# Kernel optimization log

Measured on AMD Instinct MI355X. Metric: run time of the kernel, lower is better.

Reference implementation:

```python
import jax, jax.numpy as jnp
import numpy as np

N = 100000      # n_nodes
D = 64          # in_features == out_features (elementwise W mul requires equality)
DEG = 16        # avg degree for random edges
H = 2           # n_head
ALPHA = 0.2     # LeakyReLU negative slope


def setup_inputs() -> dict:
    key = jax.random.key(0)
    k1, k2, k3 = jax.random.split(key, 3)
    inputs = jax.random.normal(k1, (N, D), dtype=jnp.float32)
    # random edges + self-loops so every row has at least one edge (nonzero rowsum)
    rnd = jax.random.randint(k2, (2, N * DEG), 0, N)
    self_loops = jnp.tile(jnp.arange(N)[None, :], (2, 1))
    edge_index = jnp.concatenate([self_loops, rnd], axis=1)  # [2, 1.7M]
    # per-head params, matching torch init: W = ones, a ~ U(-stdv, stdv)
    W = jnp.ones((H, D), dtype=jnp.float32)
    stdv = 1.0 / np.sqrt(D * 2)
    a = jax.random.uniform(k3, (H, 2 * D), dtype=jnp.float32, minval=-stdv, maxval=stdv)
    return {"inputs": inputs, "edge_index": edge_index, "W": W, "a": a}


def reference(inputs, edge_index, W, a):
    n = inputs.shape[0]
    row, col = edge_index[0], edge_index[1]

    def head(Wh, ah):
        h = inputs * Wh  # [N, D]
        # a @ [h_src; h_dst] decomposes into per-node dots, then scalar edge gather
        score = (h @ ah[:D])[row] + (h @ ah[D:])[col]          # [E]
        e = jnp.exp(jnp.where(score > 0, score, ALPHA * score))  # exp(leaky_relu)
        rowsum = jax.ops.segment_sum(e, row, num_segments=n)     # [N]
        # sparse.mm(coo(edge, e), inputs): h_prime[i] = sum_j e_ij * inputs[j]
        h_prime = jax.ops.segment_sum(e[:, None] * inputs[col], row, num_segments=n)
        return h_prime / rowsum[:, None]

    outs = jax.vmap(head)(W, a)  # [H, N, D]
    return outs.mean(axis=0)
```

## Files before the change

kernel.cpp:

```cpp
#include <hip/hip_runtime.h>


#define D 64
#define ALPHA 0.2f
#define CAP 96
#define BSHIFT 9
#define BROWS 512
#define MAXBUK 256
#define TILE 2048
#define PACKSHIFT 23
#define COLMASK ((1u << PACKSHIFT) - 1u)

__device__ __forceinline__ unsigned bf16rne(float f) {
    unsigned u = __float_as_uint(f);
    u += 0x7fffu + ((u >> 16) & 1u);
    return u >> 16;
}

__global__ __launch_bounds__(256) void k_scores_cast(
    const float* __restrict__ x, const float* __restrict__ W,
    const float* __restrict__ a, float4* __restrict__ s,
    unsigned short* __restrict__ xh, int N)
{
    int wid  = (blockIdx.x * blockDim.x + threadIdx.x) >> 6;
    int lane = threadIdx.x & 63;
    if (wid >= N) return;
    float v = x[(size_t)wid * D + lane];
    xh[(size_t)wid * D + lane] = (unsigned short)bf16rne(v);
    float h0 = v * W[lane];
    float h1 = v * W[D + lane];
    float t0 = h0 * a[lane];
    float t1 = h0 * a[D + lane];
    float t2 = h1 * a[2 * D + lane];
    float t3 = h1 * a[3 * D + lane];
#pragma unroll
    for (int off = 32; off; off >>= 1) {
        t0 += __shfl_xor(t0, off);
        t1 += __shfl_xor(t1, off);
        t2 += __shfl_xor(t2, off);
        t3 += __shfl_xor(t3, off);
    }
    if (lane == 0) s[wid] = make_float4(t0, t1, t2, t3);
}

__global__ __launch_bounds__(256) void k_tile_hist(
    const int* __restrict__ row, unsigned short* __restrict__ tcnt, int E, int nbuk)
{
    __shared__ int h[MAXBUK];
    int t = threadIdx.x, base = blockIdx.x * TILE;
    int cnt = E - base; if (cnt > TILE) cnt = TILE;
    for (int i = t; i < nbuk; i += 256) h[i] = 0;
    __syncthreads();
    for (int i = t; i < cnt; i += 256) atomicAdd(&h[row[base + i] >> BSHIFT], 1);
    __syncthreads();
    for (int i = t; i < nbuk; i += 256)
        tcnt[(size_t)blockIdx.x * MAXBUK + i] = (unsigned short)h[i];
}

__global__ __launch_bounds__(256) void k_col_scan(
    const unsigned short* __restrict__ tcnt, int* __restrict__ tbase,
    int* __restrict__ bcnt, int NT, int nbuk)
{
    __shared__ int wsum[256];
    int b = blockIdx.x, t = threadIdx.x;
    int t4 = t * 4;
    int v0 = (t4     < NT) ? tcnt[(size_t)(t4    ) * MAXBUK + b] : 0;
    int v1 = (t4 + 1 < NT) ? tcnt[(size_t)(t4 + 1) * MAXBUK + b] : 0;
    int v2 = (t4 + 2 < NT) ? tcnt[(size_t)(t4 + 2) * MAXBUK + b] : 0;
    int v3 = (t4 + 3 < NT) ? tcnt[(size_t)(t4 + 3) * MAXBUK + b] : 0;
    int sv = v0 + v1 + v2 + v3;
    wsum[t] = sv;
    __syncthreads();
    for (int off = 1; off < 256; off <<= 1) {
        int add = (t >= off) ? wsum[t - off] : 0;
        __syncthreads();
        wsum[t] += add;
        __syncthreads();
    }
    int run = wsum[t] - sv;
    if (t4     < NT) { tbase[(t4    ) * MAXBUK + b] = run; run += v0; }
    if (t4 + 1 < NT) { tbase[(t4 + 1) * MAXBUK + b] = run; run += v1; }
    if (t4 + 2 < NT) { tbase[(t4 + 2) * MAXBUK + b] = run; run += v2; }
    if (t4 + 3 < NT) { tbase[(t4 + 3) * MAXBUK + b] = run; run += v3; }
    if (t == 255) bcnt[b] = wsum[255];
}

__global__ void k_bucket_scan(const int* __restrict__ bcnt,
                              int* __restrict__ bbase, int nbuk)
{
    __shared__ int sd[MAXBUK];
    int t = threadIdx.x;
    int v = (t < nbuk) ? bcnt[t] : 0;
    sd[t] = v;
    __syncthreads();
    for (int off = 1; off < MAXBUK; off <<= 1) {
        int add = (t >= off) ? sd[t - off] : 0;
        __syncthreads();
        sd[t] += add;
        __syncthreads();
    }
    if (t < nbuk) bbase[t] = sd[t] - v;
    if (t == nbuk - 1) bbase[nbuk] = sd[t];
}

__global__ __launch_bounds__(256) void k_binning(
    const int* __restrict__ row, const int* __restrict__ col,
    const int* __restrict__ bbase, const int* __restrict__ tbase,
    unsigned* __restrict__ ebuf, int E, int nbuk)
{
    __shared__ int lrow[TILE];
    __shared__ int lcol[TILE];
    __shared__ int h[MAXBUK];
    __shared__ int st[MAXBUK];
    __shared__ int gb[MAXBUK];
    __shared__ int cur[MAXBUK];
    __shared__ int sd[MAXBUK];
    int t = threadIdx.x;
    int base = blockIdx.x * TILE;
    int cnt = E - base; if (cnt > TILE) cnt = TILE;

    for (int i = t; i < nbuk; i += 256) h[i] = 0;
    __syncthreads();

    int r[8], c[8], b[8];
#pragma unroll
    for (int j = 0; j < 8; j++) {
        int li = j * 256 + t;
        if (li < cnt) {
            int idx = base + li;
            r[j] = row[idx]; c[j] = col[idx]; b[j] = r[j] >> BSHIFT;
            atomicAdd(&h[b[j]], 1);
        } else b[j] = -1;
    }
    __syncthreads();

    sd[t] = (t < nbuk) ? h[t] : 0;
    __syncthreads();
    for (int off = 1; off < MAXBUK; off <<= 1) {
        int add = (t >= off) ? sd[t - off] : 0;
        __syncthreads();
        sd[t] += add;
        __syncthreads();
    }
    if (t < nbuk) {
        int start = sd[t] - h[t];
        st[t]  = start;
        cur[t] = start;
        gb[t]  = bbase[t] + tbase[blockIdx.x * MAXBUK + t];
    }
    __syncthreads();

#pragma unroll
    for (int j = 0; j < 8; j++) {
        if (b[j] >= 0) {
            int p = atomicAdd(&cur[b[j]], 1);
            lrow[p] = r[j]; lcol[p] = c[j];
        }
    }
    __syncthreads();

    for (int i = t; i < cnt; i += 256) {
        int rr = lrow[i];
        int bb = rr >> BSHIFT;
        ebuf[gb[bb] + (i - st[bb])] =
            ((unsigned)(rr & (BROWS - 1)) << PACKSHIFT) | (unsigned)lcol[i];
    }
}

__global__ __launch_bounds__(1024) void k_rowsort(
    const unsigned* __restrict__ ebuf, const int* __restrict__ bbase,
    int* __restrict__ offsets, int* __restrict__ counts,
    int* __restrict__ scol, int N)
{
    __shared__ int hist[BROWS];
    __shared__ int offs[BROWS];
    __shared__ int wsum[256];
    int b = blockIdx.x, t = threadIdx.x;
    int lo = b << BSHIFT;
    int s0 = bbase[b], s1 = bbase[b + 1];

    if (t < BROWS) hist[t] = 0;
    __syncthreads();
    for (int i = s0 + t; i < s1; i += 1024)
        atomicAdd(&hist[ebuf[i] >> PACKSHIFT], 1);
    __syncthreads();

    int a0 = 0, a1 = 0, sv = 0;
    if (t < 256) { a0 = hist[2 * t]; a1 = hist[2 * t + 1]; sv = a0 + a1; wsum[t] = sv; }
    __syncthreads();
    for (int off = 1; off < 256; off <<= 1) {
        int add = 0;
        if (t < 256 && t >= off) add = wsum[t - off];
        __syncthreads();
        if (t < 256) wsum[t] += add;
        __syncthreads();
    }
    if (t < 256) { int run = wsum[t] - sv; offs[2 * t] = run; offs[2 * t + 1] = run + a0; }
    __syncthreads();

    if (t < BROWS) {
        int rg = lo + t;
        if (rg < N) { offsets[rg] = s0 + offs[t]; counts[rg] = hist[t]; }
    }
    __syncthreads();
    if (t < BROWS) hist[t] = offs[t];
    __syncthreads();

    for (int i = s0 + t; i < s1; i += 1024) {
        unsigned pk = ebuf[i];
        int p = atomicAdd(&hist[pk >> PACKSHIFT], 1);
        scol[s0 + p] = (int)(pk & COLMASK);
    }
}

__global__ __launch_bounds__(256) void k_gather(
    const unsigned* __restrict__ xh2, const float4* __restrict__ s,
    const int* __restrict__ offsets, const int* __restrict__ counts,
    const int* __restrict__ scol, float* __restrict__ out, int N)
{
    __shared__ float  le0[4][CAP];
    __shared__ float  le1[4][CAP];
    __shared__ float2 lpair[4][CAP];
    int w    = threadIdx.x >> 6;
    int lane = threadIdx.x & 63;
    int n    = blockIdx.x * 4 + w;
    bool valid = (n < N);
    int start = 0, cnt = 0;
    float4 srow = make_float4(0.f, 0.f, 0.f, 0.f);
    if (valid) { start = offsets[n]; cnt = counts[n]; srow = s[n]; }

    float sum0 = 0.f, sum1 = 0.f;
    for (int k = lane; k < cnt; k += 64) {
        int c = scol[start + k];
        float4 sc = s[c];
        float sc0 = srow.x + sc.y;
        float sc1 = srow.z + sc.w;
        float e0 = __expf(sc0 > 0.f ? sc0 : ALPHA * sc0);
        float e1 = __expf(sc1 > 0.f ? sc1 : ALPHA * sc1);
        sum0 += e0; sum1 += e1;
        if (k < CAP) { lpair[w][k].x = __int_as_float(c); le0[w][k] = e0; le1[w][k] = e1; }
    }
    int m  = cnt < CAP ? cnt : CAP;
    int mp = (m + 7) & ~7;
    {
        int k = m + lane;
        if (k < mp) { lpair[w][k].x = __int_as_float(0); le0[w][k] = 0.f; le1[w][k] = 0.f; }
    }
#pragma unroll
    for (int off = 32; off; off >>= 1) {
        sum0 += __shfl_xor(sum0, off);
        sum1 += __shfl_xor(sum1, off);
    }
    if (!valid) return;
    float inv0 = 0.5f / sum0, inv1 = 0.5f / sum1;
    for (int k = lane; k < mp; k += 64)
        lpair[w][k].y = inv0 * le0[w][k] + inv1 * le1[w][k];

    int half = lane >> 5;
    int li   = lane & 31;
    float acc0 = 0.f, acc1 = 0.f;
    for (int k = 0; k < mp; k += 8) {
#pragma unroll
        for (int j = 0; j < 4; j++) {
            int kk = k + 2 * j + half;
            float2 pr = lpair[w][kk];
            int c = __float_as_int(pr.x);
            unsigned u = xh2[((unsigned)c << 5) + li];
            acc0 += pr.y * __uint_as_float(u << 16);
            acc1 += pr.y * __uint_as_float(u & 0xffff0000u);
        }
    }
    for (int kk = CAP + half; kk < cnt; kk += 2) {
        int c = scol[start + kk];
        float4 sc = s[c];
        float sc0 = srow.x + sc.y, sc1 = srow.z + sc.w;
        float coef = inv0 * __expf(sc0 > 0.f ? sc0 : ALPHA * sc0)
                   + inv1 * __expf(sc1 > 0.f ? sc1 : ALPHA * sc1);
        unsigned u = xh2[((unsigned)c << 5) + li];
        acc0 += coef * __uint_as_float(u << 16);
        acc1 += coef * __uint_as_float(u & 0xffff0000u);
    }
    acc0 += __shfl_xor(acc0, 32);
    acc1 += __shfl_xor(acc1, 32);
    if (half == 0) {
        float2* o = (float2*)(out + (size_t)n * D);
        o[li] = make_float2(acc0, acc1);
    }
}

extern "C" void kernel_launch(void* const* d_in, const int* in_sizes, int n_in,
                              void* d_out, int out_size, void* d_ws, size_t ws_size,
                              hipStream_t stream)
{
    const float* x  = (const float*)d_in[0];
    const int*   ei = (const int*)d_in[1];
    const float* W  = (const float*)d_in[2];
    const float* a  = (const float*)d_in[3];
    float*       out = (float*)d_out;
    int N = in_sizes[0] / D;
    int E = in_sizes[1] / 2;
    const int* row = ei;
    const int* col = ei + E;

    int NBUK = (N + BROWS - 1) >> BSHIFT;
    int NT   = (E + TILE - 1) / TILE;

    uintptr_t wp = (uintptr_t)d_ws;
    auto alloc = [&wp](size_t bytes) -> void* {
        wp = (wp + 255) & ~(uintptr_t)255;
        void* p = (void*)wp;
        wp += bytes;
        return p;
    };
    unsigned short* xh      = (unsigned short*)alloc((size_t)N * D * 2);
    float4*         s       = (float4*)alloc((size_t)N * sizeof(float4));
    int*            offsets = (int*)alloc((size_t)N * sizeof(int));
    int*            counts  = (int*)alloc((size_t)N * sizeof(int));
    int*            scol    = (int*)alloc((size_t)E * sizeof(int));
    unsigned*       ebuf    = (unsigned*)alloc((size_t)E * sizeof(unsigned));
    int*            tbase   = (int*)alloc((size_t)NT * MAXBUK * sizeof(int));
    int*            bcnt    = (int*)alloc(MAXBUK * sizeof(int));
    int*            bbase   = (int*)alloc((MAXBUK + 4) * sizeof(int));
    unsigned short* tcnt    = (unsigned short*)alloc((size_t)NT * MAXBUK * 2);

    k_scores_cast<<<(N + 3) / 4, 256, 0, stream>>>(x, W, a, s, xh, N);
    k_tile_hist<<<NT, 256, 0, stream>>>(row, tcnt, E, NBUK);
    k_col_scan<<<NBUK, 256, 0, stream>>>(tcnt, tbase, bcnt, NT, NBUK);
    k_bucket_scan<<<1, MAXBUK, 0, stream>>>(bcnt, bbase, NBUK);
    k_binning<<<NT, 256, 0, stream>>>(row, col, bbase, tbase, ebuf, E, NBUK);
    k_rowsort<<<NBUK, 1024, 0, stream>>>(ebuf, bbase, offsets, counts, scol, N);
    k_gather<<<(N + 3) / 4, 256, 0, stream>>>((const unsigned*)xh, s, offsets, counts, scol, out, N);
}
```

Measured before the change: 185.6 us.

## Fuse cast with histogram, drop bucket-scan kernel, widen gather loads

Merges the score/cast kernel and the tile histogram into one launch, and removes the single-block bucket scan by redoing that scan inside the binning and rowsort kernels. Scores are split into separate src/dst float2 arrays so the per-edge gather reads 8 bytes instead of 16. The aggregation loop now has each lane load a 16-byte uint4 (8 bf16 features), with 8 edges handled in parallel per wavefront and a shuffle reduction at the end. This cuts launch count and per-edge memory traffic, at the cost of more registers and redundant scans in every block.

```diff
diff --git a/kernel.cpp b/kernel.cpp
--- a/kernel.cpp
+++ b/kernel.cpp
@@ -17,12 +17,26 @@
     return u >> 16;
 }
 
-__global__ __launch_bounds__(256) void k_scores_cast(
+__global__ __launch_bounds__(256) void k_cast_hist(
     const float* __restrict__ x, const float* __restrict__ W,
-    const float* __restrict__ a, float4* __restrict__ s,
-    unsigned short* __restrict__ xh, int N)
-{
-    int wid  = (blockIdx.x * blockDim.x + threadIdx.x) >> 6;
+    const float* __restrict__ a, float2* __restrict__ ssrc,
+    float2* __restrict__ sdst, unsigned short* __restrict__ xh, int N,
+    const int* __restrict__ row, unsigned short* __restrict__ tcnt,
+    int E, int nbuk, int NT)
+{
+    if ((int)blockIdx.x < NT) {
+        __shared__ int h[MAXBUK];
+        int t = threadIdx.x, base = blockIdx.x * TILE;
+        int cnt = E - base; if (cnt > TILE) cnt = TILE;
+        for (int i = t; i < nbuk; i += 256) h[i] = 0;
+        __syncthreads();
+        for (int i = t; i < cnt; i += 256) atomicAdd(&h[row[base + i] >> BSHIFT], 1);
+        __syncthreads();
+        for (int i = t; i < nbuk; i += 256)
+            tcnt[(size_t)blockIdx.x * MAXBUK + i] = (unsigned short)h[i];
+        return;
+    }
+    int wid  = (blockIdx.x - NT) * 4 + (threadIdx.x >> 6);
     int lane = threadIdx.x & 63;
     if (wid >= N) return;
     float v = x[(size_t)wid * D + lane];
@@ -40,21 +54,7 @@
         t2 += __shfl_xor(t2, off);
         t3 += __shfl_xor(t3, off);
     }
-    if (lane == 0) s[wid] = make_float4(t0, t1, t2, t3);
-}
-
-__global__ __launch_bounds__(256) void k_tile_hist(
-    const int* __restrict__ row, unsigned short* __restrict__ tcnt, int E, int nbuk)
-{
-    __shared__ int h[MAXBUK];
-    int t = threadIdx.x, base = blockIdx.x * TILE;
-    int cnt = E - base; if (cnt > TILE) cnt = TILE;
-    for (int i = t; i < nbuk; i += 256) h[i] = 0;
-    __syncthreads();
-    for (int i = t; i < cnt; i += 256) atomicAdd(&h[row[base + i] >> BSHIFT], 1);
-    __syncthreads();
-    for (int i = t; i < nbuk; i += 256)
-        tcnt[(size_t)blockIdx.x * MAXBUK + i] = (unsigned short)h[i];
+    if (lane == 0) { ssrc[wid] = make_float2(t0, t2); sdst[wid] = make_float2(t1, t3); }
 }
 
 __global__ __launch_bounds__(256) void k_col_scan(
@@ -85,27 +85,9 @@
     if (t == 255) bcnt[b] = wsum[255];
 }
 
-__global__ void k_bucket_scan(const int* __restrict__ bcnt,
-                              int* __restrict__ bbase, int nbuk)
-{
-    __shared__ int sd[MAXBUK];
-    int t = threadIdx.x;
-    int v = (t < nbuk) ? bcnt[t] : 0;
-    sd[t] = v;
-    __syncthreads();
-    for (int off = 1; off < MAXBUK; off <<= 1) {
-        int add = (t >= off) ? sd[t - off] : 0;
-        __syncthreads();
-        sd[t] += add;
-        __syncthreads();
-    }
-    if (t < nbuk) bbase[t] = sd[t] - v;
-    if (t == nbuk - 1) bbase[nbuk] = sd[t];
-}
-
 __global__ __launch_bounds__(256) void k_binning(
     const int* __restrict__ row, const int* __restrict__ col,
-    const int* __restrict__ bbase, const int* __restrict__ tbase,
+    const int* __restrict__ bcnt, const int* __restrict__ tbase,
     unsigned* __restrict__ ebuf, int E, int nbuk)
 {
     __shared__ int lrow[TILE];
@@ -115,6 +97,7 @@
     __shared__ int gb[MAXBUK];
     __shared__ int cur[MAXBUK];
     __shared__ int sd[MAXBUK];
+    __shared__ int sb[MAXBUK];
     int t = threadIdx.x;
     int base = blockIdx.x * TILE;
     int cnt = E - base; if (cnt > TILE) cnt = TILE;
@@ -134,19 +117,23 @@
     }
     __syncthreads();
 
+    int bv = (t < nbuk) ? bcnt[t] : 0;
     sd[t] = (t < nbuk) ? h[t] : 0;
+    sb[t] = bv;
     __syncthreads();
     for (int off = 1; off < MAXBUK; off <<= 1) {
-        int add = (t >= off) ? sd[t - off] : 0;
+        int add  = (t >= off) ? sd[t - off] : 0;
+        int add2 = (t >= off) ? sb[t - off] : 0;
         __syncthreads();
         sd[t] += add;
+        sb[t] += add2;
         __syncthreads();
     }
     if (t < nbuk) {
         int start = sd[t] - h[t];
         st[t]  = start;
         cur[t] = start;
-        gb[t]  = bbase[t] + tbase[blockIdx.x * MAXBUK + t];
+        gb[t]  = (sb[t] - bv) + tbase[blockIdx.x * MAXBUK + t];
     }
     __syncthreads();
 
@@ -168,19 +155,29 @@
 }
 
 __global__ __launch_bounds__(1024) void k_rowsort(
-    const unsigned* __restrict__ ebuf, const int* __restrict__ bbase,
+    const unsigned* __restrict__ ebuf, const int* __restrict__ bcnt,
     int* __restrict__ offsets, int* __restrict__ counts,
-    int* __restrict__ scol, int N)
+    int* __restrict__ scol, int N, int nbuk)
 {
     __shared__ int hist[BROWS];
     __shared__ int offs[BROWS];
     __shared__ int wsum[256];
+    __shared__ int bsc[MAXBUK];
     int b = blockIdx.x, t = threadIdx.x;
     int lo = b << BSHIFT;
-    int s0 = bbase[b], s1 = bbase[b + 1];
-
+
+    if (t < MAXBUK) bsc[t] = (t < nbuk) ? bcnt[t] : 0;
     if (t < BROWS) hist[t] = 0;
     __syncthreads();
+    for (int off = 1; off < MAXBUK; off <<= 1) {
+        int add = (t < MAXBUK && t >= off) ? bsc[t - off] : 0;
+        __syncthreads();
+        if (t < MAXBUK) bsc[t] += add;
+        __syncthreads();
+    }
+    int s1 = bsc[b];
+    int s0 = s1 - bcnt[b];
+
     for (int i = s0 + t; i < s1; i += 1024)
         atomicAdd(&hist[ebuf[i] >> PACKSHIFT], 1);
     __syncthreads();
@@ -214,7 +211,8 @@
 }
 
 __global__ __launch_bounds__(256) void k_gather(
-    const unsigned* __restrict__ xh2, const float4* __restrict__ s,
+    const uint4* __restrict__ xh4, const float2* __restrict__ ssrc,
+    const float2* __restrict__ sdst,
     const int* __restrict__ offsets, const int* __restrict__ counts,
     const int* __restrict__ scol, float* __restrict__ out, int N)
 {
@@ -226,15 +224,15 @@
     int n    = blockIdx.x * 4 + w;
     bool valid = (n < N);
     int start = 0, cnt = 0;
-    float4 srow = make_float4(0.f, 0.f, 0.f, 0.f);
-    if (valid) { start = offsets[n]; cnt = counts[n]; srow = s[n]; }
+    float2 srow = make_float2(0.f, 0.f);
+    if (valid) { start = offsets[n]; cnt = counts[n]; srow = ssrc[n]; }
 
     float sum0 = 0.f, sum1 = 0.f;
     for (int k = lane; k < cnt; k += 64) {
         int c = scol[start + k];
-        float4 sc = s[c];
-        float sc0 = srow.x + sc.y;
-        float sc1 = srow.z + sc.w;
+        float2 sd = sdst[c];
+        float sc0 = srow.x + sd.x;
+        float sc1 = srow.y + sd.y;
         float e0 = __expf(sc0 > 0.f ? sc0 : ALPHA * sc0);
         float e1 = __expf(sc1 > 0.f ? sc1 : ALPHA * sc1);
         sum0 += e0; sum1 += e1;
@@ -256,35 +254,51 @@
     for (int k = lane; k < mp; k += 64)
         lpair[w][k].y = inv0 * le0[w][k] + inv1 * le1[w][k];
 
-    int half = lane >> 5;
-    int li   = lane & 31;
-    float acc0 = 0.f, acc1 = 0.f;
+    int e  = lane >> 3;
+    int fi = lane & 7;
+    float a0 = 0.f, a1 = 0.f, a2 = 0.f, a3 = 0.f;
+    float a4 = 0.f, a5 = 0.f, a6 = 0.f, a7 = 0.f;
     for (int k = 0; k < mp; k += 8) {
-#pragma unroll
-        for (int j = 0; j < 4; j++) {
-            int kk = k + 2 * j + half;
-            float2 pr = lpair[w][kk];
-            int c = __float_as_int(pr.x);
-            unsigned u = xh2[((unsigned)c << 5) + li];
-            acc0 += pr.y * __uint_as_float(u << 16);
-            acc1 += pr.y * __uint_as_float(u & 0xffff0000u);
-        }
-    }
-    for (int kk = CAP + half; kk < cnt; kk += 2) {
+        float2 pr = lpair[w][k + e];
+        int c = __float_as_int(pr.x);
+        uint4 u = xh4[((unsigned)c << 3) + fi];
+        float cf = pr.y;
+        a0 += cf * __uint_as_float(u.x << 16);
+        a1 += cf * __uint_as_float(u.x & 0xffff0000u);
+        a2 += cf * __uint_as_float(u.y << 16);
+        a3 += cf * __uint_as_float(u.y & 0xffff0000u);
+        a4 += cf * __uint_as_float(u.z << 16);
+        a5 += cf * __uint_as_float(u.z & 0xffff0000u);
+        a6 += cf * __uint_as_float(u.w << 16);
+        a7 += cf * __uint_as_float(u.w & 0xffff0000u);
+    }
+    for (int kk = CAP + e; kk < cnt; kk += 8) {
         int c = scol[start + kk];
-        float4 sc = s[c];
-        float sc0 = srow.x + sc.y, sc1 = srow.z + sc.w;
+        float2 sd = sdst[c];
+        float sc0 = srow.x + sd.x, sc1 = srow.y + sd.y;
         float coef = inv0 * __expf(sc0 > 0.f ? sc0 : ALPHA * sc0)
                    + inv1 * __expf(sc1 > 0.f ? sc1 : ALPHA * sc1);
-        unsigned u = xh2[((unsigned)c << 5) + li];
-        acc0 += coef * __uint_as_float(u << 16);
-        acc1 += coef * __uint_as_float(u & 0xffff0000u);
-    }
-    acc0 += __shfl_xor(acc0, 32);
-    acc1 += __shfl_xor(acc1, 32);
-    if (half == 0) {
-        float2* o = (float2*)(out + (size_t)n * D);
-        o[li] = make_float2(acc0, acc1);
+        uint4 u = xh4[((unsigned)c << 3) + fi];
+        a0 += coef * __uint_as_float(u.x << 16);
+        a1 += coef * __uint_as_float(u.x & 0xffff0000u);
+        a2 += coef * __uint_as_float(u.y << 16);
+        a3 += coef * __uint_as_float(u.y & 0xffff0000u);
+        a4 += coef * __uint_as_float(u.z << 16);
+        a5 += coef * __uint_as_float(u.z & 0xffff0000u);
+        a6 += coef * __uint_as_float(u.w << 16);
+        a7 += coef * __uint_as_float(u.w & 0xffff0000u);
+    }
+#pragma unroll
+    for (int off = 8; off < 64; off <<= 1) {
+        a0 += __shfl_xor(a0, off); a1 += __shfl_xor(a1, off);
+        a2 += __shfl_xor(a2, off); a3 += __shfl_xor(a3, off);
+        a4 += __shfl_xor(a4, off); a5 += __shfl_xor(a5, off);
+        a6 += __shfl_xor(a6, off); a7 += __shfl_xor(a7, off);
+    }
+    if (e == 0) {
+        float4* o = (float4*)(out + (size_t)n * D + (fi << 3));
+        o[0] = make_float4(a0, a1, a2, a3);
+        o[1] = make_float4(a4, a5, a6, a7);
     }
 }
 
@@ -313,21 +327,22 @@
         return p;
     };
     unsigned short* xh      = (unsigned short*)alloc((size_t)N * D * 2);
-    float4*         s       = (float4*)alloc((size_t)N * sizeof(float4));
+    float2*         ssrc    = (float2*)alloc((size_t)N * sizeof(float2));
+    float2*         sdst    = (float2*)alloc((size_t)N * sizeof(float2));
     int*            offsets = (int*)alloc((size_t)N * sizeof(int));
     int*            counts  = (int*)alloc((size_t)N * sizeof(int));
     int*            scol    = (int*)alloc((size_t)E * sizeof(int));
     unsigned*       ebuf    = (unsigned*)alloc((size_t)E * sizeof(unsigned));
     int*            tbase   = (int*)alloc((size_t)NT * MAXBUK * sizeof(int));
     int*            bcnt    = (int*)alloc(MAXBUK * sizeof(int));
-    int*            bbase   = (int*)alloc((MAXBUK + 4) * sizeof(int));
     unsigned short* tcnt    = (unsigned short*)alloc((size_t)NT * MAXBUK * 2);
 
-    k_scores_cast<<<(N + 3) / 4, 256, 0, stream>>>(x, W, a, s, xh, N);
-    k_tile_hist<<<NT, 256, 0, stream>>>(row, tcnt, E, NBUK);
+    int grid_ch = NT + (N + 3) / 4;
+    k_cast_hist<<<grid_ch, 256, 0, stream>>>(x, W, a, ssrc, sdst, xh, N,
+                                             row, tcnt, E, NBUK, NT);
     k_col_scan<<<NBUK, 256, 0, stream>>>(tcnt, tbase, bcnt, NT, NBUK);
-    k_bucket_scan<<<1, MAXBUK, 0, stream>>>(bcnt, bbase, NBUK);
-    k_binning<<<NT, 256, 0, stream>>>(row, col, bbase, tbase, ebuf, E, NBUK);
-    k_rowsort<<<NBUK, 1024, 0, stream>>>(ebuf, bbase, offsets, counts, scol, N);
-    k_gather<<<(N + 3) / 4, 256, 0, stream>>>((const unsigned*)xh, s, offsets, counts, scol, out, N);
-}
+    k_binning<<<NT, 256, 0, stream>>>(row, col, bcnt, tbase, ebuf, E, NBUK);
+    k_rowsort<<<NBUK, 1024, 0, stream>>>(ebuf, bcnt, offsets, counts, scol, N, NBUK);
+    k_gather<<<(N + 3) / 4, 256, 0, stream>>>((const uint4*)xh, ssrc, sdst,
+                                              offsets, counts, scol, out, N);
+}
```

Result: slower. 192.7 us (+3.8%).

## Replace bucket sort with atomic per-edge scoring and scatter into CSR pairs

Applied to the files above, without the earlier changes.

Drops the tile histogram, bucket binning and per-bucket row sort, replacing them with two edge-parallel passes. The first pass atomically accumulates per-row softmax sums and degrees. A two-level scan follows, and the second pass computes normalized coefficients and scatters (col, coef) pairs into CSR order through atomic row cursors. The gather kernel then just streams the pairs, and x is stored as fp16 instead of bf16. This trades sort-structured local memory work for global atomics and random scatter writes, and makes the edge order within each row nondeterministic.

```diff
diff --git a/kernel.cpp b/kernel.cpp
--- a/kernel.cpp
+++ b/kernel.cpp
@@ -1,32 +1,26 @@
 #include <hip/hip_runtime.h>
+#include <hip/hip_fp16.h>
 
 
 #define D 64
 #define ALPHA 0.2f
-#define CAP 96
-#define BSHIFT 9
-#define BROWS 512
-#define MAXBUK 256
-#define TILE 2048
-#define PACKSHIFT 23
-#define COLMASK ((1u << PACKSHIFT) - 1u)
 
-__device__ __forceinline__ unsigned bf16rne(float f) {
-    unsigned u = __float_as_uint(f);
-    u += 0x7fffu + ((u >> 16) & 1u);
-    return u >> 16;
-}
-
-__global__ __launch_bounds__(256) void k_scores_cast(
+__global__ __launch_bounds__(256) void k_scores(
     const float* __restrict__ x, const float* __restrict__ W,
-    const float* __restrict__ a, float4* __restrict__ s,
-    unsigned short* __restrict__ xh, int N)
+    const float* __restrict__ a, float2* __restrict__ ssrc,
+    float2* __restrict__ sdst, __half* __restrict__ xh,
+    int4* __restrict__ zero4, int zwords4, int ZBLK, int N)
 {
-    int wid  = (blockIdx.x * blockDim.x + threadIdx.x) >> 6;
+    if ((int)blockIdx.x < ZBLK) {
+        int i = blockIdx.x * 256 + threadIdx.x;
+        if (i < zwords4) zero4[i] = make_int4(0, 0, 0, 0);
+        return;
+    }
+    int wid  = (blockIdx.x - ZBLK) * 4 + (threadIdx.x >> 6);
     int lane = threadIdx.x & 63;
     if (wid >= N) return;
     float v = x[(size_t)wid * D + lane];
-    xh[(size_t)wid * D + lane] = (unsigned short)bf16rne(v);
+    xh[(size_t)wid * D + lane] = __float2half(v);
     float h0 = v * W[lane];
     float h1 = v * W[D + lane];
     float t0 = h0 * a[lane];
@@ -40,245 +34,110 @@
         t2 += __shfl_xor(t2, off);
         t3 += __shfl_xor(t3, off);
     }
-    if (lane == 0) s[wid] = make_float4(t0, t1, t2, t3);
+    if (lane == 0) { ssrc[wid] = make_float2(t0, t2); sdst[wid] = make_float2(t1, t3); }
 }
 
-__global__ __launch_bounds__(256) void k_tile_hist(
-    const int* __restrict__ row, unsigned short* __restrict__ tcnt, int E, int nbuk)
+__global__ __launch_bounds__(256) void k_edge1(
+    const int* __restrict__ row, const int* __restrict__ col,
+    const float2* __restrict__ ssrc, const float2* __restrict__ sdst,
+    float* __restrict__ rowsum, int* __restrict__ cnt, int E)
 {
-    __shared__ int h[MAXBUK];
-    int t = threadIdx.x, base = blockIdx.x * TILE;
-    int cnt = E - base; if (cnt > TILE) cnt = TILE;
-    for (int i = t; i < nbuk; i += 256) h[i] = 0;
-    __syncthreads();
-    for (int i = t; i < cnt; i += 256) atomicAdd(&h[row[base + i] >> BSHIFT], 1);
-    __syncthreads();
-    for (int i = t; i < nbuk; i += 256)
-        tcnt[(size_t)blockIdx.x * MAXBUK + i] = (unsigned short)h[i];
+    int i = blockIdx.x * 256 + threadIdx.x;
+    if (i >= E) return;
+    int r = row[i], c = col[i];
+    float2 sa = ssrc[r], sb = sdst[c];
+    float sc0 = sa.x + sb.x, sc1 = sa.y + sb.y;
+    float e0 = __expf(sc0 > 0.f ? sc0 : ALPHA * sc0);
+    float e1 = __expf(sc1 > 0.f ? sc1 : ALPHA * sc1);
+    atomicAdd(&rowsum[2 * r],     e0);
+    atomicAdd(&rowsum[2 * r + 1], e1);
+    atomicAdd(&cnt[r], 1);
 }
 
-__global__ __launch_bounds__(256) void k_col_scan(
-    const unsigned short* __restrict__ tcnt, int* __restrict__ tbase,
-    int* __restrict__ bcnt, int NT, int nbuk)
+__global__ __launch_bounds__(256) void k_scan_a(
+    const int* __restrict__ cnt, const float2* __restrict__ rowsum2,
+    int* __restrict__ offs, int* __restrict__ bsum,
+    float2* __restrict__ invrs)
 {
-    __shared__ int wsum[256];
+    __shared__ int ws[256];
     int b = blockIdx.x, t = threadIdx.x;
-    int t4 = t * 4;
-    int v0 = (t4     < NT) ? tcnt[(size_t)(t4    ) * MAXBUK + b] : 0;
-    int v1 = (t4 + 1 < NT) ? tcnt[(size_t)(t4 + 1) * MAXBUK + b] : 0;
-    int v2 = (t4 + 2 < NT) ? tcnt[(size_t)(t4 + 2) * MAXBUK + b] : 0;
-    int v3 = (t4 + 3 < NT) ? tcnt[(size_t)(t4 + 3) * MAXBUK + b] : 0;
-    int sv = v0 + v1 + v2 + v3;
-    wsum[t] = sv;
+    int i = b * 256 + t;
+    int v = cnt[i];
+    ws[t] = v;
     __syncthreads();
     for (int off = 1; off < 256; off <<= 1) {
-        int add = (t >= off) ? wsum[t - off] : 0;
+        int add = (t >= off) ? ws[t - off] : 0;
         __syncthreads();
-        wsum[t] += add;
+        ws[t] += add;
         __syncthreads();
     }
-    int run = wsum[t] - sv;
-    if (t4     < NT) { tbase[(t4    ) * MAXBUK + b] = run; run += v0; }
-    if (t4 + 1 < NT) { tbase[(t4 + 1) * MAXBUK + b] = run; run += v1; }
-    if (t4 + 2 < NT) { tbase[(t4 + 2) * MAXBUK + b] = run; run += v2; }
-    if (t4 + 3 < NT) { tbase[(t4 + 3) * MAXBUK + b] = run; run += v3; }
-    if (t == 255) bcnt[b] = wsum[255];
+    offs[i] = ws[t] - v;
+    if (t == 255) bsum[b] = ws[255];
+    float2 rs = rowsum2[i];
+    invrs[i] = make_float2(0.5f / rs.x, 0.5f / rs.y);
 }
 
-__global__ void k_bucket_scan(const int* __restrict__ bcnt,
-                              int* __restrict__ bbase, int nbuk)
+__global__ __launch_bounds__(512) void k_scan_b(int* __restrict__ bsum, int nb)
 {
-    __shared__ int sd[MAXBUK];
+    __shared__ int ws[512];
     int t = threadIdx.x;
-    int v = (t < nbuk) ? bcnt[t] : 0;
-    sd[t] = v;
+    int v = (t < nb) ? bsum[t] : 0;
+    ws[t] = v;
     __syncthreads();
-    for (int off = 1; off < MAXBUK; off <<= 1) {
-        int add = (t >= off) ? sd[t - off] : 0;
+    for (int off = 1; off < 512; off <<= 1) {
+        int add = (t >= off) ? ws[t - off] : 0;
         __syncthreads();
-        sd[t] += add;
+        ws[t] += add;
         __syncthreads();
     }
-    if (t < nbuk) bbase[t] = sd[t] - v;
-    if (t == nbuk - 1) bbase[nbuk] = sd[t];
+    if (t < nb) bsum[t] = ws[t] - v;
 }
 
-__global__ __launch_bounds__(256) void k_binning(
+__global__ __launch_bounds__(256) void k_edge2(
     const int* __restrict__ row, const int* __restrict__ col,
-    const int* __restrict__ bbase, const int* __restrict__ tbase,
-    unsigned* __restrict__ ebuf, int E, int nbuk)
+    const float2* __restrict__ ssrc, const float2* __restrict__ sdst,
+    const float2* __restrict__ invrs, const int* __restrict__ bsum,
+    int* __restrict__ offs, float2* __restrict__ pairs, int E)
 {
-    __shared__ int lrow[TILE];
-    __shared__ int lcol[TILE];
-    __shared__ int h[MAXBUK];
-    __shared__ int st[MAXBUK];
-    __shared__ int gb[MAXBUK];
-    __shared__ int cur[MAXBUK];
-    __shared__ int sd[MAXBUK];
-    int t = threadIdx.x;
-    int base = blockIdx.x * TILE;
-    int cnt = E - base; if (cnt > TILE) cnt = TILE;
-
-    for (int i = t; i < nbuk; i += 256) h[i] = 0;
-    __syncthreads();
-
-    int r[8], c[8], b[8];
-#pragma unroll
-    for (int j = 0; j < 8; j++) {
-        int li = j * 256 + t;
-        if (li < cnt) {
-            int idx = base + li;
-            r[j] = row[idx]; c[j] = col[idx]; b[j] = r[j] >> BSHIFT;
-            atomicAdd(&h[b[j]], 1);
-        } else b[j] = -1;
-    }
-    __syncthreads();
-
-    sd[t] = (t < nbuk) ? h[t] : 0;
-    __syncthreads();
-    for (int off = 1; off < MAXBUK; off <<= 1) {
-        int add = (t >= off) ? sd[t - off] : 0;
-        __syncthreads();
-        sd[t] += add;
-        __syncthreads();
-    }
-    if (t < nbuk) {
-        int start = sd[t] - h[t];
-        st[t]  = start;
-        cur[t] = start;
-        gb[t]  = bbase[t] + tbase[blockIdx.x * MAXBUK + t];
-    }
-    __syncthreads();
-
-#pragma unroll
-    for (int j = 0; j < 8; j++) {
-        if (b[j] >= 0) {
-            int p = atomicAdd(&cur[b[j]], 1);
-            lrow[p] = r[j]; lcol[p] = c[j];
-        }
-    }
-    __syncthreads();
-
-    for (int i = t; i < cnt; i += 256) {
-        int rr = lrow[i];
-        int bb = rr >> BSHIFT;
-        ebuf[gb[bb] + (i - st[bb])] =
-            ((unsigned)(rr & (BROWS - 1)) << PACKSHIFT) | (unsigned)lcol[i];
-    }
-}
-
-__global__ __launch_bounds__(1024) void k_rowsort(
-    const unsigned* __restrict__ ebuf, const int* __restrict__ bbase,
-    int* __restrict__ offsets, int* __restrict__ counts,
-    int* __restrict__ scol, int N)
-{
-    __shared__ int hist[BROWS];
-    __shared__ int offs[BROWS];
-    __shared__ int wsum[256];
-    int b = blockIdx.x, t = threadIdx.x;
-    int lo = b << BSHIFT;
-    int s0 = bbase[b], s1 = bbase[b + 1];
-
-    if (t < BROWS) hist[t] = 0;
-    __syncthreads();
-    for (int i = s0 + t; i < s1; i += 1024)
-        atomicAdd(&hist[ebuf[i] >> PACKSHIFT], 1);
-    __syncthreads();
-
-    int a0 = 0, a1 = 0, sv = 0;
-    if (t < 256) { a0 = hist[2 * t]; a1 = hist[2 * t + 1]; sv = a0 + a1; wsum[t] = sv; }
-    __syncthreads();
-    for (int off = 1; off < 256; off <<= 1) {
-        int add = 0;
-        if (t < 256 && t >= off) add = wsum[t - off];
-        __syncthreads();
-        if (t < 256) wsum[t] += add;
-        __syncthreads();
-    }
-    if (t < 256) { int run = wsum[t] - sv; offs[2 * t] = run; offs[2 * t + 1] = run + a0; }
-    __syncthreads();
-
-    if (t < BROWS) {
-        int rg = lo + t;
-        if (rg < N) { offsets[rg] = s0 + offs[t]; counts[rg] = hist[t]; }
-    }
-    __syncthreads();
-    if (t < BROWS) hist[t] = offs[t];
-    __syncthreads();
-
-    for (int i = s0 + t; i < s1; i += 1024) {
-        unsigned pk = ebuf[i];
-        int p = atomicAdd(&hist[pk >> PACKSHIFT], 1);
-        scol[s0 + p] = (int)(pk & COLMASK);
-    }
+    int i = blockIdx.x * 256 + threadIdx.x;
+    if (i >= E) return;
+    int r = row[i], c = col[i];
+    float2 sa = ssrc[r], sb = sdst[c];
+    float sc0 = sa.x + sb.x, sc1 = sa.y + sb.y;
+    float e0 = __expf(sc0 > 0.f ? sc0 : ALPHA * sc0);
+    float e1 = __expf(sc1 > 0.f ? sc1 : ALPHA * sc1);
+    float2 iv = invrs[r];
+    float cf = e0 * iv.x + e1 * iv.y;
+    int p = atomicAdd(&offs[r], 1);
+    pairs[bsum[r >> 8] + p] = make_float2(__int_as_float(c), cf);
 }
 
 __global__ __launch_bounds__(256) void k_gather(
-    const unsigned* __restrict__ xh2, const float4* __restrict__ s,
-    const int* __restrict__ offsets, const int* __restrict__ counts,
-    const int* __restrict__ scol, float* __restrict__ out, int N)
+    const unsigned* __restrict__ xhd, const float2* __restrict__ pairs,
+    const int* __restrict__ offs, const int* __restrict__ cnt,
+    const int* __restrict__ bsum, float* __restrict__ out, int N)
 {
-    __shared__ float  le0[4][CAP];
-    __shared__ float  le1[4][CAP];
-    __shared__ float2 lpair[4][CAP];
     int w    = threadIdx.x >> 6;
     int lane = threadIdx.x & 63;
     int n    = blockIdx.x * 4 + w;
-    bool valid = (n < N);
-    int start = 0, cnt = 0;
-    float4 srow = make_float4(0.f, 0.f, 0.f, 0.f);
-    if (valid) { start = offsets[n]; cnt = counts[n]; srow = s[n]; }
-
-    float sum0 = 0.f, sum1 = 0.f;
-    for (int k = lane; k < cnt; k += 64) {
-        int c = scol[start + k];
-        float4 sc = s[c];
-        float sc0 = srow.x + sc.y;
-        float sc1 = srow.z + sc.w;
-        float e0 = __expf(sc0 > 0.f ? sc0 : ALPHA * sc0);
-        float e1 = __expf(sc1 > 0.f ? sc1 : ALPHA * sc1);
-        sum0 += e0; sum1 += e1;
-        if (k < CAP) { lpair[w][k].x = __int_as_float(c); le0[w][k] = e0; le1[w][k] = e1; }
-    }
-    int m  = cnt < CAP ? cnt : CAP;
-    int mp = (m + 7) & ~7;
-    {
-        int k = m + lane;
-        if (k < mp) { lpair[w][k].x = __int_as_float(0); le0[w][k] = 0.f; le1[w][k] = 0.f; }
-    }
-#pragma unroll
-    for (int off = 32; off; off >>= 1) {
-        sum0 += __shfl_xor(sum0, off);
-        sum1 += __shfl_xor(sum1, off);
-    }
-    if (!valid) return;
-    float inv0 = 0.5f / sum0, inv1 = 0.5f / sum1;
-    for (int k = lane; k < mp; k += 64)
-        lpair[w][k].y = inv0 * le0[w][k] + inv1 * le1[w][k];
-
-    int half = lane >> 5;
-    int li   = lane & 31;
+    if (n >= N) return;
+    int cl    = cnt[n];
+    int start = bsum[n >> 8] + offs[n] - cl;
+    int half  = lane >> 5;
+    int li    = lane & 31;
     float acc0 = 0.f, acc1 = 0.f;
-    for (int k = 0; k < mp; k += 8) {
-#pragma unroll
-        for (int j = 0; j < 4; j++) {
-            int kk = k + 2 * j + half;
-            float2 pr = lpair[w][kk];
-            int c = __float_as_int(pr.x);
-            unsigned u = xh2[((unsigned)c << 5) + li];
-            acc0 += pr.y * __uint_as_float(u << 16);
-            acc1 += pr.y * __uint_as_float(u & 0xffff0000u);
-        }
-    }
-    for (int kk = CAP + half; kk < cnt; kk += 2) {
-        int c = scol[start + kk];
-        float4 sc = s[c];
-        float sc0 = srow.x + sc.y, sc1 = srow.z + sc.w;
-        float coef = inv0 * __expf(sc0 > 0.f ? sc0 : ALPHA * sc0)
-                   + inv1 * __expf(sc1 > 0.f ? sc1 : ALPHA * sc1);
-        unsigned u = xh2[((unsigned)c << 5) + li];
-        acc0 += coef * __uint_as_float(u << 16);
-        acc1 += coef * __uint_as_float(u & 0xffff0000u);
+    for (int k = 0; k < cl; k += 4) {
+        int j0 = k + half, j1 = k + 2 + half;
+        float2 p0 = pairs[start + (j0 < cl ? j0 : cl - 1)];
+        float2 p1 = pairs[start + (j1 < cl ? j1 : cl - 1)];
+        float cf0 = (j0 < cl) ? p0.y : 0.f;
+        float cf1 = (j1 < cl) ? p1.y : 0.f;
+        unsigned u0 = xhd[((unsigned)__float_as_int(p0.x) << 5) + li];
+        unsigned u1 = xhd[((unsigned)__float_as_int(p1.x) << 5) + li];
+        float2 f0 = __half22float2(*(__half2*)&u0);
+        float2 f1 = __half22float2(*(__half2*)&u1);
+        acc0 += cf0 * f0.x; acc1 += cf0 * f0.y;
+        acc0 += cf1 * f1.x; acc1 += cf1 * f1.y;
     }
     acc0 += __shfl_xor(acc0, 32);
     acc1 += __shfl_xor(acc1, 32);
@@ -302,8 +161,8 @@
     const int* row = ei;
     const int* col = ei + E;
 
-    int NBUK = (N + BROWS - 1) >> BSHIFT;
-    int NT   = (E + TILE - 1) / TILE;
+    int NB2  = (N + 255) / 256;
+    int NPAD = NB2 * 256;
 
     uintptr_t wp = (uintptr_t)d_ws;
     auto alloc = [&wp](size_t bytes) -> void* {
@@ -312,22 +171,28 @@
         wp += bytes;
         return p;
     };
-    unsigned short* xh      = (unsigned short*)alloc((size_t)N * D * 2);
-    float4*         s       = (float4*)alloc((size_t)N * sizeof(float4));
-    int*            offsets = (int*)alloc((size_t)N * sizeof(int));
-    int*            counts  = (int*)alloc((size_t)N * sizeof(int));
-    int*            scol    = (int*)alloc((size_t)E * sizeof(int));
-    unsigned*       ebuf    = (unsigned*)alloc((size_t)E * sizeof(unsigned));
-    int*            tbase   = (int*)alloc((size_t)NT * MAXBUK * sizeof(int));
-    int*            bcnt    = (int*)alloc(MAXBUK * sizeof(int));
-    int*            bbase   = (int*)alloc((MAXBUK + 4) * sizeof(int));
-    unsigned short* tcnt    = (unsigned short*)alloc((size_t)NT * MAXBUK * 2);
+    __half* xh     = (__half*)alloc((size_t)N * D * 2);
+    float2* ssrc   = (float2*)alloc((size_t)N * sizeof(float2));
+    float2* sdst   = (float2*)alloc((size_t)N * sizeof(float2));
+    float*  rowsum = (float*)alloc((size_t)NPAD * 2 * sizeof(float));
+    int*    cntb   = (int*)alloc((size_t)NPAD * sizeof(int));
+    float2* invrs  = (float2*)alloc((size_t)NPAD * sizeof(float2));
+    int*    offs   = (int*)alloc((size_t)NPAD * sizeof(int));
+    int*    bsum   = (int*)alloc(512 * sizeof(int));
+    float2* pairs  = (float2*)alloc((size_t)E * sizeof(float2));
 
-    k_scores_cast<<<(N + 3) / 4, 256, 0, stream>>>(x, W, a, s, xh, N);
-    k_tile_hist<<<NT, 256, 0, stream>>>(row, tcnt, E, NBUK);
-    k_col_scan<<<NBUK, 256, 0, stream>>>(tcnt, tbase, bcnt, NT, NBUK);
-    k_bucket_scan<<<1, MAXBUK, 0, stream>>>(bcnt, bbase, NBUK);
-    k_binning<<<NT, 256, 0, stream>>>(row, col, bbase, tbase, ebuf, E, NBUK);
-    k_rowsort<<<NBUK, 1024, 0, stream>>>(ebuf, bbase, offsets, counts, scol, N);
-    k_gather<<<(N + 3) / 4, 256, 0, stream>>>((const unsigned*)xh, s, offsets, counts, scol, out, N);
+    size_t zbytes  = (size_t)((char*)cntb - (char*)rowsum) + (size_t)NPAD * 4;
+    int    zwords4 = (int)(zbytes / 16);
+    int    ZBLK    = (zwords4 + 255) / 256;
+
+    int EB = (E + 255) / 256;
+
+    k_scores<<<ZBLK + (N + 3) / 4, 256, 0, stream>>>(
+        x, W, a, ssrc, sdst, xh, (int4*)rowsum, zwords4, ZBLK, N);
+    k_edge1<<<EB, 256, 0, stream>>>(row, col, ssrc, sdst, rowsum, cntb, E);
+    k_scan_a<<<NB2, 256, 0, stream>>>(cntb, (const float2*)rowsum, offs, bsum, invrs);
+    k_scan_b<<<1, 512, 0, stream>>>(bsum, NB2);
+    k_edge2<<<EB, 256, 0, stream>>>(row, col, ssrc, sdst, invrs, bsum, offs, pairs, E);
+    k_gather<<<(N + 3) / 4, 256, 0, stream>>>(
+        (const unsigned*)xh, pairs, offs, cntb, bsum, out, N);
 }
```

New measurement: 470.2 us. 2.53x slower.
